# Kernel tuning notes

Hardware: AMD Instinct MI355X
Metric: run time of the kernel (lower is better)

## Reference

```python
import jax, jax.numpy as jnp
import numpy as np

B, S, E = 2, 4096, 1024
QD, VD = 64, 64
WIN, DIL = 5, 2


def setup_inputs() -> dict:
    key = jax.random.key(0)
    ks = jax.random.split(key, 7)
    sc = E ** -0.5  # linear-layer init scale
    return {
        "x": jax.random.normal(ks[0], (B, S, E), jnp.float32),
        "Wq": jax.random.normal(ks[1], (E, QD), jnp.float32) * sc,
        "bq": jnp.zeros((QD,), jnp.float32),
        "Wk": jax.random.normal(ks[2], (E, QD), jnp.float32) * sc,
        "bk": jnp.zeros((QD,), jnp.float32),
        "Wv": jax.random.normal(ks[3], (E, VD), jnp.float32) * sc,
        "bv": jnp.zeros((VD,), jnp.float32),
    }


def reference(x, Wq, bq, Wk, bk, Wv, bv):
    b, s, _ = x.shape
    Q = x @ Wq + bq  # (b, s, QD)
    K = x @ Wk + bk  # (b, s, QD)
    V = x @ Wv + bv  # (b, s, VD)

    half = WIN // 2
    offsets = DIL * (jnp.arange(WIN) - half)
    i = jnp.arange(s)                                  # (s,)
    j = i[None, :] + offsets[:, None]
    valid = (j >= 0) & (j < s)                         # in-range band entries
    jc = jnp.clip(j, 0, s - 1)

    Kg = K[:, jc, :]
    # per-offset diagonal dot products Q_i . K_{i+d}
    c = jnp.einsum('bsd,bwsd->bws', Q, Kg) * valid

    ib = jnp.broadcast_to(i[None, :], (WIN, s))
    # Banded score matrix, zeros off-band (as in the original: torch.zeros scatter).
    # Masked (invalid) entries add 0, so clipped index collisions are harmless.
    scores = jnp.zeros((b, s, s), x.dtype).at[:, ib, jc].add(c)

    attn = jax.nn.softmax(scores, axis=2)              # softmax over full row incl. zeros
    return attn @ V                                    # (b, s, VD)
```

## Files before the change

kernel.cpp:

```cpp
#include <hip/hip_runtime.h>
#include <hip/hip_bf16.h>

typedef __hip_bfloat16 bf16;
typedef short bf16x8 __attribute__((ext_vector_type(8)));
typedef float f32x4 __attribute__((ext_vector_type(4)));

#define S_LEN 4096
#define NBATCH 2
#define EDIM 1024
#define DDIM 64
#define MROWS (NBATCH * S_LEN)

#define GLOBAL_AS __attribute__((address_space(1)))
#define LDS_AS __attribute__((address_space(3)))

union frag_u { bf16x8 v; bf16 e[8]; };

__device__ __forceinline__ void async_ld16(const void* gp, void* lp) {
  __builtin_amdgcn_global_load_lds((const GLOBAL_AS void*)gp,
                                   (LDS_AS void*)lp, 16, 0, 0);
}

__device__ __forceinline__ void cvt_split(const float4& a, const float4& b,
                                          bf16x8& hi, bf16x8& lo) {
  float v[8] = {a.x, a.y, a.z, a.w, b.x, b.y, b.z, b.w};
  frag_u h, l;
#pragma unroll
  for (int e = 0; e < 8; e++) {
    bf16 hh = __float2bfloat16(v[e]);
    h.e[e] = hh;
    l.e[e] = __float2bfloat16(v[e] - __bfloat162float(hh));
  }
  hi = h.v;
  lo = l.v;
}

__global__ __launch_bounds__(256) void pack_w_kernel(
    const float* __restrict__ Wq, const float* __restrict__ Wk,
    const float* __restrict__ Wv, bf16* __restrict__ Wt2_hi,
    bf16* __restrict__ Wt2_lo, float* __restrict__ Vsum) {
  __shared__ float tile[64 * 65];
  const int mat = blockIdx.x >> 4;
  const int kb = blockIdx.x & 15;
  const int t = threadIdx.x;
  if (blockIdx.x == 0 && t < NBATCH * DDIM) Vsum[t] = 0.f;
  const float* W = (mat == 0) ? Wq : ((mat == 1) ? Wk : Wv);

#pragma unroll
  for (int i = 0; i < 4; i++) {
    int F = (i * 256 + t) * 4;
    int k = F >> 6;
    int n4 = F & 63;
    float4 v = *(const float4*)(const void*)(W + (size_t)(kb * 64 + k) * 64 + n4);
    tile[(n4 + 0) * 65 + k] = v.x;
    tile[(n4 + 1) * 65 + k] = v.y;
    tile[(n4 + 2) * 65 + k] = v.z;
    tile[(n4 + 3) * 65 + k] = v.w;
  }
  __syncthreads();

#pragma unroll
  for (int it = 0; it < 2; it++) {
    int uidx = it * 256 + t;
    int nl = uidx >> 3;
    int j_half = (uidx >> 2) & 1;
    int pp_k = uidx & 3;
    int ng = mat * 64 + nl;
    int n2 = ng >> 1;
    int sp = ((ng & 1) * 4 + pp_k) ^ (n2 & 7);
    int unit = n2 * 8 + sp;
    int j = kb * 2 + j_half;
    frag_u h, l;
#pragma unroll
    for (int e = 0; e < 8; e++) {
      float v = tile[nl * 65 + j_half * 32 + pp_k * 8 + e];
      bf16 hh = __float2bfloat16(v);
      h.e[e] = hh;
      l.e[e] = __float2bfloat16(v - __bfloat162float(hh));
    }
    size_t ob = (size_t)j * 6144 + unit * 8;
    *(bf16x8*)(void*)(Wt2_hi + ob) = h.v;
    *(bf16x8*)(void*)(Wt2_lo + ob) = l.v;
  }
}

__global__ __launch_bounds__(512, 2) void qkv_gemm_kernel(
    const float* __restrict__ x, const bf16* __restrict__ Wt2_hi,
    const bf16* __restrict__ Wt2_lo, const float* __restrict__ bq,
    const float* __restrict__ bk, const float* __restrict__ bv,
    float* __restrict__ qkv, float* __restrict__ Vsum) {
  __shared__ __align__(16) char lds[57344];
  const int tid = threadIdx.x;
  const int lane = tid & 63;
  const int wave = tid >> 6;
  const int quad = lane >> 4;
  const int l16 = lane & 15;
  const int mt = wave >> 2;
  const int nh = wave & 3;
  const int rowBase = blockIdx.x * 32;

  const char* gsrc[4];
  int gstride[4], ldoff[4];
  const int nch = (wave < 4) ? 4 : 3;
#pragma unroll
  for (int s = 0; s < 4; s++) {
    int c = wave + s * 8;
    ldoff[s] = c * 1024;
    if (c < 4) {
      int rin = lane >> 3;
      int part = (lane & 7) ^ rin;
      gsrc[s] = (const char*)(x + (size_t)(rowBase + c * 8 + rin) * EDIM +
                              part * 4);
      gstride[s] = 128;
    } else if (c < 16) {
      gsrc[s] = (const char*)Wt2_hi + (c - 4) * 1024 + lane * 16;
      gstride[s] = 12288;
    } else {
      gsrc[s] = (const char*)Wt2_lo + (c - 16) * 1024 + lane * 16;
      gstride[s] = 12288;
    }
  }

  f32x4 acc[3];
#pragma unroll
  for (int t = 0; t < 3; t++) acc[t] = (f32x4){0.f, 0.f, 0.f, 0.f};

#pragma unroll
  for (int s = 0; s < 4; s++)
    if (s < nch) async_ld16(gsrc[s], lds + ldoff[s]);
  __syncthreads();

  const int arow = mt * 16 + l16;
  const int asp0 = (quad * 2) ^ (l16 & 7);
  for (int j = 0; j < 32; j++) {
    const int b = j & 1;
    if (j + 1 < 32) {
      char* nb = lds + (1 - b) * 28672;
#pragma unroll
      for (int s = 0; s < 4; s++)
        if (s < nch)
          async_ld16(gsrc[s] + (size_t)(j + 1) * gstride[s], nb + ldoff[s]);
    }
    const char* Ab = lds + b * 28672;
    const bf16* Bhb = (const bf16*)(lds + b * 28672 + 4096);
    const bf16* Blb = (const bf16*)(lds + b * 28672 + 16384);
    float4 a0 = *(const float4*)(const void*)(Ab + (arow * 8 + asp0) * 16);
    float4 a1 = *(const float4*)(const void*)(Ab + (arow * 8 + (asp0 ^ 1)) * 16);
    bf16x8 ah, al;
    cvt_split(a0, a1, ah, al);
#pragma unroll
    for (int t = 0; t < 3; t++) {
      int nt = nh * 3 + t;
      int n2 = nt * 8 + (l16 >> 1);
      int sp = (((l16 & 1) * 4) + quad) ^ ((l16 >> 1) & 7);
      int uoff = (n2 * 8 + sp) * 8;
      bf16x8 bh = *(const bf16x8*)(const void*)(Bhb + uoff);
      bf16x8 bl = *(const bf16x8*)(const void*)(Blb + uoff);
      acc[t] = __builtin_amdgcn_mfma_f32_16x16x32_bf16(ah, bh, acc[t], 0, 0, 0);
      acc[t] = __builtin_amdgcn_mfma_f32_16x16x32_bf16(ah, bl, acc[t], 0, 0, 0);
      acc[t] = __builtin_amdgcn_mfma_f32_16x16x32_bf16(al, bh, acc[t], 0, 0, 0);
    }
    __syncthreads();
  }

  const int bb = rowBase >> 12;
#pragma unroll
  for (int t = 0; t < 3; t++) {
    int nt = nh * 3 + t;
    int n = nt * 16 + l16;
    int mat = n >> 6;
    int col = n & 63;
    float bias = (mat == 0) ? bq[col] : ((mat == 1) ? bk[col] : bv[col]);
    float* dst = qkv + (size_t)mat * MROWS * DDIM +
                 (size_t)(rowBase + mt * 16 + quad * 4) * DDIM + col;
    float vs = 0.f;
#pragma unroll
    for (int r = 0; r < 4; r++) {
      float val = acc[t][r] + bias;
      dst[r * DDIM] = val;
      vs += val;
    }
    if (nt >= 8) {
      vs += __shfl_xor(vs, 16, 64);
      vs += __shfl_xor(vs, 32, 64);
      if (quad == 0) atomicAdd(&Vsum[bb * DDIM + (n - 128)], vs);
    }
  }
}

__global__ __launch_bounds__(256) void attn_kernel(
    const float* __restrict__ qkv, const float* __restrict__ Vsum,
    float* __restrict__ out) {
  const float* Qf = qkv;
  const float* Kf = qkv + (size_t)MROWS * DDIM;
  const float* Vf = qkv + (size_t)2 * MROWS * DDIM;
  int l = threadIdx.x & 31;
  int qidx = blockIdx.x * 8 + (threadIdx.x >> 5);
  int b = qidx >> 12;
  int i = qidx & 4095;

  float2 q = *(const float2*)(const void*)(Qf + (size_t)qidx * DDIM + 2 * l);
  float sc[5];
  float2 vv[5];
  bool val[5];
#pragma unroll
  for (int w = 0; w < 5; w++) {
    int j = i + 2 * w - 4;
    val[w] = (j >= 0) && (j < S_LEN);
    int jj = val[w] ? j : i;
    size_t off = (size_t)(b * S_LEN + jj) * DDIM + 2 * l;
    float2 kk = *(const float2*)(const void*)(Kf + off);
    vv[w] = *(const float2*)(const void*)(Vf + off);
    float p = q.x * kk.x + q.y * kk.y;
#pragma unroll
    for (int d = 1; d < 32; d <<= 1) p += __shfl_xor(p, d, 64);
    sc[w] = p;
  }

  float mx = 0.f;
#pragma unroll
  for (int w = 0; w < 5; w++)
    if (val[w]) mx = fmaxf(mx, sc[w]);

  float denom = 0.f;
  float2 accv = {0.f, 0.f}, vsel = {0.f, 0.f};
  int nval = 0;
#pragma unroll
  for (int w = 0; w < 5; w++)
    if (val[w]) {
      float pexp = __expf(sc[w] - mx);
      denom += pexp;
      accv.x += pexp * vv[w].x;
      accv.y += pexp * vv[w].y;
      vsel.x += vv[w].x;
      vsel.y += vv[w].y;
      nval++;
    }
  float pbg = __expf(-mx);
  denom += pbg * (float)(S_LEN - nval);
  float2 vsm = *(const float2*)(const void*)(Vsum + b * DDIM + 2 * l);
  accv.x += pbg * (vsm.x - vsel.x);
  accv.y += pbg * (vsm.y - vsel.y);

  float2 o = {accv.x / denom, accv.y / denom};
  *(float2*)(void*)(out + (size_t)qidx * DDIM + 2 * l) = o;
}

extern "C" void kernel_launch(void* const* d_in, const int* in_sizes, int n_in,
                              void* d_out, int out_size, void* d_ws,
                              size_t ws_size, hipStream_t stream) {
  const float* x = (const float*)d_in[0];
  const float* Wq = (const float*)d_in[1];
  const float* bq = (const float*)d_in[2];
  const float* Wk = (const float*)d_in[3];
  const float* bk = (const float*)d_in[4];
  const float* Wv = (const float*)d_in[5];
  const float* bv = (const float*)d_in[6];
  float* out = (float*)d_out;

  char* ws = (char*)d_ws;
  bf16* Wt2_hi = (bf16*)ws;
  bf16* Wt2_lo = (bf16*)(ws + 393216);
  float* qkv = (float*)(ws + 786432);
  float* Vsum = (float*)(ws + 786432 + 6291456);

  hipLaunchKernelGGL(pack_w_kernel, dim3(48), dim3(256), 0, stream, Wq, Wk, Wv,
                     Wt2_hi, Wt2_lo, Vsum);
  hipLaunchKernelGGL(qkv_gemm_kernel, dim3(256), dim3(512), 0, stream, x,
                     Wt2_hi, Wt2_lo, bq, bk, bv, qkv, Vsum);
  hipLaunchKernelGGL(attn_kernel, dim3(1024), dim3(256), 0, stream, qkv, Vsum,
                     out);
}
```

Before: 119.0 us.

## Load weight fragments directly to registers and shrink GEMM tiles to 16 rows

The QKV GEMM now handles 16 rows per block with 4 waves, so the grid doubles to 512 blocks. Each wave now loads its bf16 hi/lo weight fragments straight from global memory into registers, double-buffered across iterations, instead of staging them in LDS. Only the x tile still goes through LDS, now a 4-deep async ring guarded by explicit vmcnt waits and a single barrier per two k-steps. This cuts LDS footprint and barrier count to raise occupancy and overlap, at the cost of more global weight traffic per row and fragile hand-coded wait counts.

```diff
diff --git a/kernel.cpp b/kernel.cpp
--- a/kernel.cpp
+++ b/kernel.cpp
@@ -84,95 +84,111 @@
   }
 }
 
-__global__ __launch_bounds__(512, 2) void qkv_gemm_kernel(
+__global__ __launch_bounds__(256, 2) void qkv_gemm_kernel(
     const float* __restrict__ x, const bf16* __restrict__ Wt2_hi,
     const bf16* __restrict__ Wt2_lo, const float* __restrict__ bq,
     const float* __restrict__ bk, const float* __restrict__ bv,
     float* __restrict__ qkv, float* __restrict__ Vsum) {
-  __shared__ __align__(16) char lds[57344];
+  __shared__ __align__(16) char lds[16384];
   const int tid = threadIdx.x;
   const int lane = tid & 63;
   const int wave = tid >> 6;
   const int quad = lane >> 4;
   const int l16 = lane & 15;
-  const int mt = wave >> 2;
-  const int nh = wave & 3;
-  const int rowBase = blockIdx.x * 32;
-
-  const char* gsrc[4];
-  int gstride[4], ldoff[4];
-  const int nch = (wave < 4) ? 4 : 3;
-#pragma unroll
-  for (int s = 0; s < 4; s++) {
-    int c = wave + s * 8;
-    ldoff[s] = c * 1024;
-    if (c < 4) {
-      int rin = lane >> 3;
-      int part = (lane & 7) ^ rin;
-      gsrc[s] = (const char*)(x + (size_t)(rowBase + c * 8 + rin) * EDIM +
-                              part * 4);
-      gstride[s] = 128;
-    } else if (c < 16) {
-      gsrc[s] = (const char*)Wt2_hi + (c - 4) * 1024 + lane * 16;
-      gstride[s] = 12288;
-    } else {
-      gsrc[s] = (const char*)Wt2_lo + (c - 16) * 1024 + lane * 16;
-      gstride[s] = 12288;
-    }
-  }
+  const int rowBase = blockIdx.x * 16;
+
+  const int rin = lane >> 3;
+  const int part = (lane & 7) ^ rin;
+  const char* aSrc = (const char*)x +
+      (size_t)(rowBase + (wave & 1) * 8 + rin) * (EDIM * 4) +
+      (wave >> 1) * 128 + part * 16;
+  char* aDstU = lds + (wave >> 1) * 2048 + (wave & 1) * 1024;
+
+  const int sp = ((l16 & 1) * 4 + quad) ^ ((l16 >> 1) & 7);
+  const int loff = ((l16 >> 1) * 8 + sp) * 8;
+  const bf16* bhp = Wt2_hi + wave * 1536 + loff;
+  const bf16* blp = Wt2_lo + wave * 1536 + loff;
 
   f32x4 acc[3];
 #pragma unroll
   for (int t = 0; t < 3; t++) acc[t] = (f32x4){0.f, 0.f, 0.f, 0.f};
 
-#pragma unroll
-  for (int s = 0; s < 4; s++)
-    if (s < nch) async_ld16(gsrc[s], lds + ldoff[s]);
-  __syncthreads();
-
-  const int arow = mt * 16 + l16;
+  async_ld16(aSrc, aDstU);
+  async_ld16(aSrc + 256, aDstU + 4096);
+  bf16x8 h0, h1, h2, l0, l1, l2, H0, H1, H2, L0, L1, L2;
+  h0 = *(const bf16x8*)(const void*)(bhp);
+  h1 = *(const bf16x8*)(const void*)(bhp + 512);
+  h2 = *(const bf16x8*)(const void*)(bhp + 1024);
+  l0 = *(const bf16x8*)(const void*)(blp);
+  l1 = *(const bf16x8*)(const void*)(blp + 512);
+  l2 = *(const bf16x8*)(const void*)(blp + 1024);
+
   const int asp0 = (quad * 2) ^ (l16 & 7);
-  for (int j = 0; j < 32; j++) {
-    const int b = j & 1;
-    if (j + 1 < 32) {
-      char* nb = lds + (1 - b) * 28672;
-#pragma unroll
-      for (int s = 0; s < 4; s++)
-        if (s < nch)
-          async_ld16(gsrc[s] + (size_t)(j + 1) * gstride[s], nb + ldoff[s]);
-    }
-    const char* Ab = lds + b * 28672;
-    const bf16* Bhb = (const bf16*)(lds + b * 28672 + 4096);
-    const bf16* Blb = (const bf16*)(lds + b * 28672 + 16384);
-    float4 a0 = *(const float4*)(const void*)(Ab + (arow * 8 + asp0) * 16);
-    float4 a1 = *(const float4*)(const void*)(Ab + (arow * 8 + (asp0 ^ 1)) * 16);
-    bf16x8 ah, al;
-    cvt_split(a0, a1, ah, al);
-#pragma unroll
-    for (int t = 0; t < 3; t++) {
-      int nt = nh * 3 + t;
-      int n2 = nt * 8 + (l16 >> 1);
-      int sp = (((l16 & 1) * 4) + quad) ^ ((l16 >> 1) & 7);
-      int uoff = (n2 * 8 + sp) * 8;
-      bf16x8 bh = *(const bf16x8*)(const void*)(Bhb + uoff);
-      bf16x8 bl = *(const bf16x8*)(const void*)(Blb + uoff);
-      acc[t] = __builtin_amdgcn_mfma_f32_16x16x32_bf16(ah, bh, acc[t], 0, 0, 0);
-      acc[t] = __builtin_amdgcn_mfma_f32_16x16x32_bf16(ah, bl, acc[t], 0, 0, 0);
-      acc[t] = __builtin_amdgcn_mfma_f32_16x16x32_bf16(al, bh, acc[t], 0, 0, 0);
-    }
-    __syncthreads();
-  }
+  const int aoff0 = (l16 * 8 + asp0) * 16;
+  const int aoff1 = (l16 * 8 + (asp0 ^ 1)) * 16;
+
+#define COMPUTE(JJ, BH0, BH1, BH2, BL0, BL1, BL2)                              \
+  {                                                                            \
+    const char* Ab = lds + (((JJ) >> 1) & 3) * 4096 + ((JJ) & 1) * 2048;       \
+    float4 a0 = *(const float4*)(const void*)(Ab + aoff0);                     \
+    float4 a1 = *(const float4*)(const void*)(Ab + aoff1);                     \
+    bf16x8 ah, al;                                                             \
+    cvt_split(a0, a1, ah, al);                                                 \
+    acc[0] = __builtin_amdgcn_mfma_f32_16x16x32_bf16(ah, BH0, acc[0], 0, 0, 0);\
+    acc[0] = __builtin_amdgcn_mfma_f32_16x16x32_bf16(ah, BL0, acc[0], 0, 0, 0);\
+    acc[0] = __builtin_amdgcn_mfma_f32_16x16x32_bf16(al, BH0, acc[0], 0, 0, 0);\
+    acc[1] = __builtin_amdgcn_mfma_f32_16x16x32_bf16(ah, BH1, acc[1], 0, 0, 0);\
+    acc[1] = __builtin_amdgcn_mfma_f32_16x16x32_bf16(ah, BL1, acc[1], 0, 0, 0);\
+    acc[1] = __builtin_amdgcn_mfma_f32_16x16x32_bf16(al, BH1, acc[1], 0, 0, 0);\
+    acc[2] = __builtin_amdgcn_mfma_f32_16x16x32_bf16(ah, BH2, acc[2], 0, 0, 0);\
+    acc[2] = __builtin_amdgcn_mfma_f32_16x16x32_bf16(ah, BL2, acc[2], 0, 0, 0);\
+    acc[2] = __builtin_amdgcn_mfma_f32_16x16x32_bf16(al, BH2, acc[2], 0, 0, 0);\
+  }
+
+  for (int j = 0; j < 32; j += 2) {
+    asm volatile("s_waitcnt vmcnt(7)" ::: "memory");
+    __builtin_amdgcn_s_barrier();
+    asm volatile("" ::: "memory");
+    {
+      const bf16* bh = bhp + (size_t)(j + 1) * 6144;
+      const bf16* bl = blp + (size_t)(j + 1) * 6144;
+      H0 = *(const bf16x8*)(const void*)(bh);
+      H1 = *(const bf16x8*)(const void*)(bh + 512);
+      H2 = *(const bf16x8*)(const void*)(bh + 1024);
+      L0 = *(const bf16x8*)(const void*)(bl);
+      L1 = *(const bf16x8*)(const void*)(bl + 512);
+      L2 = *(const bf16x8*)(const void*)(bl + 1024);
+    }
+    asm volatile("" ::: "memory");
+    if (j + 4 < 32)
+      async_ld16(aSrc + (size_t)(j / 2 + 2) * 256,
+                 aDstU + ((j / 2 + 2) & 3) * 4096);
+    COMPUTE(j, h0, h1, h2, l0, l1, l2);
+    {
+      int jn = (j + 2 < 32) ? (j + 2) : 31;
+      const bf16* bh = bhp + (size_t)jn * 6144;
+      const bf16* bl = blp + (size_t)jn * 6144;
+      h0 = *(const bf16x8*)(const void*)(bh);
+      h1 = *(const bf16x8*)(const void*)(bh + 512);
+      h2 = *(const bf16x8*)(const void*)(bh + 1024);
+      l0 = *(const bf16x8*)(const void*)(bl);
+      l1 = *(const bf16x8*)(const void*)(bl + 512);
+      l2 = *(const bf16x8*)(const void*)(bl + 1024);
+    }
+    COMPUTE(j + 1, H0, H1, H2, L0, L1, L2);
+  }
+#undef COMPUTE
 
   const int bb = rowBase >> 12;
 #pragma unroll
   for (int t = 0; t < 3; t++) {
-    int nt = nh * 3 + t;
+    int nt = wave * 3 + t;
     int n = nt * 16 + l16;
     int mat = n >> 6;
     int col = n & 63;
     float bias = (mat == 0) ? bq[col] : ((mat == 1) ? bk[col] : bv[col]);
     float* dst = qkv + (size_t)mat * MROWS * DDIM +
-                 (size_t)(rowBase + mt * 16 + quad * 4) * DDIM + col;
+                 (size_t)(rowBase + quad * 4) * DDIM + col;
     float vs = 0.f;
 #pragma unroll
     for (int r = 0; r < 4; r++) {
@@ -266,7 +282,7 @@
 
   hipLaunchKernelGGL(pack_w_kernel, dim3(48), dim3(256), 0, stream, Wq, Wk, Wv,
                      Wt2_hi, Wt2_lo, Vsum);
-  hipLaunchKernelGGL(qkv_gemm_kernel, dim3(256), dim3(512), 0, stream, x,
+  hipLaunchKernelGGL(qkv_gemm_kernel, dim3(512), dim3(256), 0, stream, x,
                      Wt2_hi, Wt2_lo, bq, bk, bv, qkv, Vsum);
   hipLaunchKernelGGL(attn_kernel, dim3(1024), dim3(256), 0, stream, qkv, Vsum,
                      out);
```

Result: faster. 109.5 us (-8.0%).

## Load GEMM operands directly to registers and split K across wave halves

Applied to the files above, without the earlier changes.

The QKV GEMM no longer stages x and packed weights through LDS with async global-to-LDS loads and per-step barriers. Each wave now reads its A and B fragments straight from global memory into registers, using a software-pipelined prefetch (B two-deep, A four-deep). The 8 waves are split into two K-halves that each cover both 16-row M tiles, and their partials are combined through a small LDS reduction at the end. This removes 32 block-wide syncs and the LDS traffic, at the cost of more register pressure and redundant global loads across waves, which now rely on the cache.

```diff
diff --git a/kernel.cpp b/kernel.cpp
--- a/kernel.cpp
+++ b/kernel.cpp
@@ -11,15 +11,7 @@
 #define DDIM 64
 #define MROWS (NBATCH * S_LEN)
 
-#define GLOBAL_AS __attribute__((address_space(1)))
-#define LDS_AS __attribute__((address_space(3)))
-
 union frag_u { bf16x8 v; bf16 e[8]; };
-
-__device__ __forceinline__ void async_ld16(const void* gp, void* lp) {
-  __builtin_amdgcn_global_load_lds((const GLOBAL_AS void*)gp,
-                                   (LDS_AS void*)lp, 16, 0, 0);
-}
 
 __device__ __forceinline__ void cvt_split(const float4& a, const float4& b,
                                           bf16x8& hi, bf16x8& lo) {
@@ -89,103 +81,122 @@
     const bf16* __restrict__ Wt2_lo, const float* __restrict__ bq,
     const float* __restrict__ bk, const float* __restrict__ bv,
     float* __restrict__ qkv, float* __restrict__ Vsum) {
-  __shared__ __align__(16) char lds[57344];
+  __shared__ f32x4 red[4][64][6];
   const int tid = threadIdx.x;
   const int lane = tid & 63;
   const int wave = tid >> 6;
+  const int nh = wave & 3;
+  const int kh = wave >> 2;
   const int quad = lane >> 4;
   const int l16 = lane & 15;
-  const int mt = wave >> 2;
-  const int nh = wave & 3;
   const int rowBase = blockIdx.x * 32;
 
-  const char* gsrc[4];
-  int gstride[4], ldoff[4];
-  const int nch = (wave < 4) ? 4 : 3;
-#pragma unroll
-  for (int s = 0; s < 4; s++) {
-    int c = wave + s * 8;
-    ldoff[s] = c * 1024;
-    if (c < 4) {
-      int rin = lane >> 3;
-      int part = (lane & 7) ^ rin;
-      gsrc[s] = (const char*)(x + (size_t)(rowBase + c * 8 + rin) * EDIM +
-                              part * 4);
-      gstride[s] = 128;
-    } else if (c < 16) {
-      gsrc[s] = (const char*)Wt2_hi + (c - 4) * 1024 + lane * 16;
-      gstride[s] = 12288;
-    } else {
-      gsrc[s] = (const char*)Wt2_lo + (c - 16) * 1024 + lane * 16;
-      gstride[s] = 12288;
-    }
-  }
-
-  f32x4 acc[3];
-#pragma unroll
-  for (int t = 0; t < 3; t++) acc[t] = (f32x4){0.f, 0.f, 0.f, 0.f};
-
-#pragma unroll
-  for (int s = 0; s < 4; s++)
-    if (s < nch) async_ld16(gsrc[s], lds + ldoff[s]);
+  const int sp = ((l16 & 1) * 4 + quad) ^ ((l16 >> 1) & 7);
+  const int loff = ((l16 >> 1) * 8 + sp) * 8;
+  const bf16* bhp = Wt2_hi + (size_t)kh * 98304 + nh * 1536 + loff;
+  const bf16* blp = Wt2_lo + (size_t)kh * 98304 + nh * 1536 + loff;
+
+  const char* aB0 = (const char*)x + (size_t)(rowBase + l16) * 4096 +
+                    kh * 2048 + quad * 32;
+  const char* aB1 = aB0 + 16 * 4096;
+
+  float4 Ab[4][2][2];
+  bf16x8 Bh[2][3], Bl[2][3];
+  f32x4 acc[2][3];
+#pragma unroll
+  for (int f = 0; f < 2; f++)
+#pragma unroll
+    for (int t = 0; t < 3; t++) acc[f][t] = (f32x4){0.f, 0.f, 0.f, 0.f};
+
+#define LOADB(s, r)                                                          \
+  {                                                                          \
+    const bf16* _h = bhp + (r) * 6144;                                       \
+    const bf16* _l = blp + (r) * 6144;                                       \
+    Bh[s][0] = *(const bf16x8*)(const void*)(_h);                            \
+    Bh[s][1] = *(const bf16x8*)(const void*)(_h + 512);                      \
+    Bh[s][2] = *(const bf16x8*)(const void*)(_h + 1024);                     \
+    Bl[s][0] = *(const bf16x8*)(const void*)(_l);                            \
+    Bl[s][1] = *(const bf16x8*)(const void*)(_l + 512);                      \
+    Bl[s][2] = *(const bf16x8*)(const void*)(_l + 1024);                     \
+  }
+#define LOADA(s, r)                                                          \
+  {                                                                          \
+    Ab[s][0][0] = *(const float4*)(const void*)(aB0 + (r) * 128);            \
+    Ab[s][0][1] = *(const float4*)(const void*)(aB0 + (r) * 128 + 16);       \
+    Ab[s][1][0] = *(const float4*)(const void*)(aB1 + (r) * 128);            \
+    Ab[s][1][1] = *(const float4*)(const void*)(aB1 + (r) * 128 + 16);       \
+  }
+
+  LOADB(0, 0);
+  LOADA(0, 0);
+  LOADA(1, 1);
+  LOADA(2, 2);
+
+#pragma unroll
+  for (int r = 0; r < 16; ++r) {
+    if (r + 1 < 16) LOADB((r + 1) & 1, r + 1);
+    if (r + 3 < 16) LOADA((r + 3) & 3, r + 3);
+    bf16x8 ah0, al0, ah1, al1;
+    cvt_split(Ab[r & 3][0][0], Ab[r & 3][0][1], ah0, al0);
+    cvt_split(Ab[r & 3][1][0], Ab[r & 3][1][1], ah1, al1);
+    const int s = r & 1;
+#pragma unroll
+    for (int t = 0; t < 3; t++) {
+      acc[0][t] =
+          __builtin_amdgcn_mfma_f32_16x16x32_bf16(ah0, Bh[s][t], acc[0][t], 0, 0, 0);
+      acc[0][t] =
+          __builtin_amdgcn_mfma_f32_16x16x32_bf16(ah0, Bl[s][t], acc[0][t], 0, 0, 0);
+      acc[0][t] =
+          __builtin_amdgcn_mfma_f32_16x16x32_bf16(al0, Bh[s][t], acc[0][t], 0, 0, 0);
+      acc[1][t] =
+          __builtin_amdgcn_mfma_f32_16x16x32_bf16(ah1, Bh[s][t], acc[1][t], 0, 0, 0);
+      acc[1][t] =
+          __builtin_amdgcn_mfma_f32_16x16x32_bf16(ah1, Bl[s][t], acc[1][t], 0, 0, 0);
+      acc[1][t] =
+          __builtin_amdgcn_mfma_f32_16x16x32_bf16(al1, Bh[s][t], acc[1][t], 0, 0, 0);
+    }
+  }
+#undef LOADA
+#undef LOADB
+
+  if (kh == 1) {
+#pragma unroll
+    for (int f = 0; f < 2; f++)
+#pragma unroll
+      for (int t = 0; t < 3; t++) red[nh][lane][f * 3 + t] = acc[f][t];
+  }
   __syncthreads();
-
-  const int arow = mt * 16 + l16;
-  const int asp0 = (quad * 2) ^ (l16 & 7);
-  for (int j = 0; j < 32; j++) {
-    const int b = j & 1;
-    if (j + 1 < 32) {
-      char* nb = lds + (1 - b) * 28672;
-#pragma unroll
-      for (int s = 0; s < 4; s++)
-        if (s < nch)
-          async_ld16(gsrc[s] + (size_t)(j + 1) * gstride[s], nb + ldoff[s]);
-    }
-    const char* Ab = lds + b * 28672;
-    const bf16* Bhb = (const bf16*)(lds + b * 28672 + 4096);
-    const bf16* Blb = (const bf16*)(lds + b * 28672 + 16384);
-    float4 a0 = *(const float4*)(const void*)(Ab + (arow * 8 + asp0) * 16);
-    float4 a1 = *(const float4*)(const void*)(Ab + (arow * 8 + (asp0 ^ 1)) * 16);
-    bf16x8 ah, al;
-    cvt_split(a0, a1, ah, al);
+  if (kh == 1) return;
+#pragma unroll
+  for (int f = 0; f < 2; f++)
+#pragma unroll
+    for (int t = 0; t < 3; t++) acc[f][t] += red[nh][lane][f * 3 + t];
+
+  const int bb = rowBase >> 12;
+#pragma unroll
+  for (int f = 0; f < 2; f++)
 #pragma unroll
     for (int t = 0; t < 3; t++) {
       int nt = nh * 3 + t;
-      int n2 = nt * 8 + (l16 >> 1);
-      int sp = (((l16 & 1) * 4) + quad) ^ ((l16 >> 1) & 7);
-      int uoff = (n2 * 8 + sp) * 8;
-      bf16x8 bh = *(const bf16x8*)(const void*)(Bhb + uoff);
-      bf16x8 bl = *(const bf16x8*)(const void*)(Blb + uoff);
-      acc[t] = __builtin_amdgcn_mfma_f32_16x16x32_bf16(ah, bh, acc[t], 0, 0, 0);
-      acc[t] = __builtin_amdgcn_mfma_f32_16x16x32_bf16(ah, bl, acc[t], 0, 0, 0);
-      acc[t] = __builtin_amdgcn_mfma_f32_16x16x32_bf16(al, bh, acc[t], 0, 0, 0);
-    }
-    __syncthreads();
-  }
-
-  const int bb = rowBase >> 12;
-#pragma unroll
-  for (int t = 0; t < 3; t++) {
-    int nt = nh * 3 + t;
-    int n = nt * 16 + l16;
-    int mat = n >> 6;
-    int col = n & 63;
-    float bias = (mat == 0) ? bq[col] : ((mat == 1) ? bk[col] : bv[col]);
-    float* dst = qkv + (size_t)mat * MROWS * DDIM +
-                 (size_t)(rowBase + mt * 16 + quad * 4) * DDIM + col;
-    float vs = 0.f;
-#pragma unroll
-    for (int r = 0; r < 4; r++) {
-      float val = acc[t][r] + bias;
-      dst[r * DDIM] = val;
-      vs += val;
-    }
-    if (nt >= 8) {
-      vs += __shfl_xor(vs, 16, 64);
-      vs += __shfl_xor(vs, 32, 64);
-      if (quad == 0) atomicAdd(&Vsum[bb * DDIM + (n - 128)], vs);
-    }
-  }
+      int n = nt * 16 + l16;
+      int mat = n >> 6;
+      int col = n & 63;
+      float bias = (mat == 0) ? bq[col] : ((mat == 1) ? bk[col] : bv[col]);
+      float* dst = qkv + (size_t)mat * MROWS * DDIM +
+                   (size_t)(rowBase + f * 16 + quad * 4) * DDIM + col;
+      float vs = 0.f;
+#pragma unroll
+      for (int rr = 0; rr < 4; rr++) {
+        float val = acc[f][t][rr] + bias;
+        dst[rr * DDIM] = val;
+        vs += val;
+      }
+      if (nt >= 8) {
+        vs += __shfl_xor(vs, 16, 64);
+        vs += __shfl_xor(vs, 32, 64);
+        if (quad == 0) atomicAdd(&Vsum[bb * DDIM + (n - 128)], vs);
+      }
+    }
 }
 
 __global__ __launch_bounds__(256) void attn_kernel(
```

After: 113.3 us. 1.05x faster.
